# Kernel optimization log

Measured on AMD Instinct MI355X. Metric: run time of the kernel, lower is better.

Reference implementation:

```python
import jax, jax.numpy as jnp
import numpy as np

N = 400_000   # active voxels
C = 128       # inplanes = outplanes
K = 9         # nplanes*3*3 kernel offsets (nplanes=1)
EPS = 1e-4    # scn BatchNormalization default eps


def setup_inputs() -> dict:
    key = jax.random.key(0)
    ks = jax.random.split(key, 5)
    feat = jax.random.normal(ks[0], (N, C), dtype=jnp.float32)
    # rulebook: neighbor active-site index per kernel offset, plus validity mask
    nbr_idx = jax.random.randint(ks[1], (N, K), 0, N, dtype=jnp.int32)
    nbr_idx = nbr_idx.at[:, K // 2].set(jnp.arange(N, dtype=jnp.int32))  # center = self
    nbr_mask = jax.random.uniform(ks[2], (N, K)) < 0.6
    nbr_mask = nbr_mask.at[:, K // 2].set(True)
    scale = 1.0 / np.sqrt(K * C)
    W1 = jax.random.normal(ks[3], (K, C, C), dtype=jnp.float32) * scale
    W2 = jax.random.normal(ks[4], (K, C, C), dtype=jnp.float32) * scale
    gamma1 = jnp.ones((C,), jnp.float32)
    beta1 = jnp.zeros((C,), jnp.float32)
    gamma2 = jnp.ones((C,), jnp.float32)
    beta2 = jnp.zeros((C,), jnp.float32)
    return {"feat": feat, "W1": W1, "W2": W2,
            "gamma1": gamma1, "beta1": beta1,
            "gamma2": gamma2, "beta2": beta2,
            "nbr_idx": nbr_idx, "nbr_mask": nbr_mask}


def _subm_conv(feat, nbr_idx, nbr_mask, W):
    # rulebook gather -> GEMM -> accumulate; output lives at the same active sites
    out = jnp.zeros((feat.shape[0], W.shape[2]), feat.dtype)
    for k in range(W.shape[0]):  # small fixed K=9 structural loop
        xk = jnp.where(nbr_mask[:, k:k + 1], feat[nbr_idx[:, k]], 0.0)
        out = out + xk @ W[k]
    return out


def _batchnorm(x, gamma, beta):
    mu = jnp.mean(x, axis=0)
    var = jnp.mean(jnp.square(x - mu), axis=0)
    return (x - mu) * (gamma * jax.lax.rsqrt(var + EPS)) + beta


def reference(feat, W1, W2, gamma1, beta1, gamma2, beta2, nbr_idx, nbr_mask):
    residual = feat                                   # scn.Identity (stride=1)
    out = _subm_conv(feat, nbr_idx, nbr_mask, W1)     # conv1
    out = jax.nn.relu(_batchnorm(out, gamma1, beta1))  # BatchNormReLU
    out = _subm_conv(out, nbr_idx, nbr_mask, W2)      # conv2
    out = _batchnorm(out, gamma2, beta2)              # bn2
    return jax.nn.relu(out + residual)                # AddTable + ReLU
```

## Files before the change

kernel.cpp:

```cpp
#include <hip/hip_runtime.h>


#define C_CH 128
#define K_OFF 9
#define MTILE 64

typedef __attribute__((ext_vector_type(8))) short bf16x8;
typedef __attribute__((ext_vector_type(4))) float f32x4;
typedef __attribute__((ext_vector_type(8))) unsigned short u16x8;

typedef __attribute__((address_space(1))) const unsigned int* gas_p;
typedef __attribute__((address_space(3))) unsigned int* las_p;

__device__ __forceinline__ void gload_lds16(const unsigned short* g, unsigned short* l) {
    __builtin_amdgcn_global_load_lds((gas_p)g, (las_p)l, 16, 0, 0);
}

__device__ __forceinline__ unsigned short f2b(float f) {
    union { float f; unsigned u; } v; v.f = f;
    unsigned r = v.u + 0x7fffu + ((v.u >> 16) & 1u);
    return (unsigned short)(r >> 16);
}
__device__ __forceinline__ float b2f(unsigned short h) {
    union { unsigned u; float f; } v; v.u = ((unsigned)h) << 16;
    return v.f;
}


__global__ void init_k(float* stats, unsigned int* zrow1, unsigned int* zrow2) {
    int t = threadIdx.x;
    if (t < 512) stats[t] = 0.f;
    if (t >= 512 && t < 514) ((int*)stats)[1024 + (t - 512)] = 0;
    if (t < 64) { zrow1[t] = 0u; zrow2[t] = 0u; }
}

__global__ void detect_mask_k(const unsigned char* __restrict__ m, int* flagA, int* flagB) {
    int i = blockIdx.x * blockDim.x + threadIdx.x;
    unsigned char v = m[i];
    if ((i & 3) != 0 && v != 0) atomicOr(flagA, 1);
    if (v > 1) atomicOr(flagB, 1);
}

__global__ void fold_idx_k(const int* __restrict__ nidx, const void* __restrict__ m,
                           const int* __restrict__ flagA, const int* __restrict__ flagB,
                           int* __restrict__ eidx, int n, int N) {
    int i = blockIdx.x * blockDim.x + threadIdx.x;
    if (i >= n) return;
    int fa = *flagA, fb = *flagB;
    bool t;
    if (!fa)       t = ((const int*)m)[i] != 0;
    else if (fb)   t = ((const unsigned*)m)[i] != 0;
    else           t = ((const unsigned char*)m)[i] != 0;
    eidx[i] = t ? nidx[i] : N;
}

__global__ void convert_feat_k(const float* __restrict__ x, unsigned short* __restrict__ y, int n4) {
    int i = blockIdx.x * blockDim.x + threadIdx.x;
    int s = gridDim.x * blockDim.x;
    for (; i < n4; i += s) {
        float4 f = ((const float4*)x)[i];
        ushort4 o;
        o.x = f2b(f.x); o.y = f2b(f.y); o.z = f2b(f.z); o.w = f2b(f.w);
        ((ushort4*)y)[i] = o;
    }
}

__global__ void pack_w_k(const float* __restrict__ W1, unsigned short* __restrict__ Wp1,
                         const float* __restrict__ W2, unsigned short* __restrict__ Wp2) {
    int i = blockIdx.x * blockDim.x + threadIdx.x;
    const int tot = K_OFF * 8 * 4 * 512;
    const float* W = (i < tot) ? W1 : W2;
    unsigned short* Wp = (i < tot) ? Wp1 : Wp2;
    int ii = (i < tot) ? i : i - tot;
    if (i >= 2 * tot) return;
    int j = ii & 7;
    int l = (ii >> 3) & 63;
    int frag = ii >> 9;
    int ks = frag & 3;
    int nt = (frag >> 2) & 7;
    int ko = frag >> 5;
    int cin = ks * 32 + (l >> 4) * 8 + j;
    int cout = nt * 16 + (l & 15);
    Wp[ii] = f2b(W[ko * C_CH * C_CH + cin * C_CH + cout]);
}


__global__ __launch_bounds__(256) void conv_kernel(
    const unsigned short* __restrict__ Xb,
    const unsigned short* __restrict__ Wp,
    const int* __restrict__ eidx,
    unsigned short* __restrict__ Yraw,
    float* __restrict__ statS, float* __restrict__ statQ)
{
    const int tid = threadIdx.x;
    const int lane = tid & 63;
    const int wv = tid >> 6;
    const int tile = blockIdx.x * MTILE;
    const int asub = lane >> 4;
    const int l15 = lane & 15;

    __shared__ alignas(16) unsigned short At[3][MTILE * C_CH];
    __shared__ int sIdxT[K_OFF][MTILE];

    for (int i = tid; i < MTILE * K_OFF; i += 256) {
        int r = i / K_OFF, k = i - r * K_OFF;
        sIdxT[k][r] = eidx[(size_t)(tile + r) * K_OFF + k];
    }
    __syncthreads();

    const int r_st = tid >> 4;
    const int ch_st = tid & 15;

    #define STAGE(buf, ko)                                                        \
        {                                                                         \
            _Pragma("unroll")                                                     \
            for (int jr = 0; jr < 4; ++jr) {                                      \
                int r = jr * 16 + r_st;                                           \
                int g = sIdxT[ko][r];                                             \
                const unsigned short* src =                                       \
                    Xb + (size_t)g * C_CH + ((ch_st ^ (r & 7)) * 8);              \
                unsigned short* dst = &At[buf][r * C_CH + ch_st * 8];             \
                gload_lds16(src, dst);                                            \
            }                                                                     \
        }

    f32x4 acc[4][2];
    #pragma unroll
    for (int m = 0; m < 4; ++m) { acc[m][0] = (f32x4){0,0,0,0}; acc[m][1] = (f32x4){0,0,0,0}; }

    STAGE(0, 0);
    STAGE(1, 1);

    #define CONV_ITER(KO, VM)                                                     \
        {                                                                         \
            bf16x8 bfrag0[4], bfrag1[4];                                          \
            const unsigned short* wb = Wp + (size_t)(KO) * (8 * 4 * 512) + lane * 8; \
            _Pragma("unroll")                                                     \
            for (int ks = 0; ks < 4; ++ks) {                                      \
                bfrag0[ks] = *(const bf16x8*)(wb + ((wv * 2 + 0) * 4 + ks) * 512);\
                bfrag1[ks] = *(const bf16x8*)(wb + ((wv * 2 + 1) * 4 + ks) * 512);\
            }                                                                     \
            __builtin_amdgcn_sched_barrier(0);                                    \
            asm volatile("s_waitcnt vmcnt(" #VM ")" ::: "memory");                \
            __builtin_amdgcn_s_barrier();                                         \
            __builtin_amdgcn_sched_barrier(0);                                    \
            if ((KO) + 2 < K_OFF) { STAGE((((KO) + 2) % 3), (KO) + 2); }          \
            _Pragma("unroll")                                                     \
            for (int m = 0; m < 4; ++m) {                                         \
                bf16x8 a[4];                                                      \
                _Pragma("unroll")                                                 \
                for (int ks = 0; ks < 4; ++ks) {                                  \
                    int row = m * 16 + l15;                                       \
                    int sc = (ks * 4 + asub) ^ (row & 7);                         \
                    a[ks] = *(const bf16x8*)((const char*)At[(KO) % 3] + row * 256 + sc * 16); \
                }                                                                 \
                _Pragma("unroll")                                                 \
                for (int ks = 0; ks < 4; ++ks) {                                  \
                    acc[m][0] = __builtin_amdgcn_mfma_f32_16x16x32_bf16(a[ks], bfrag0[ks], acc[m][0], 0, 0, 0); \
                    acc[m][1] = __builtin_amdgcn_mfma_f32_16x16x32_bf16(a[ks], bfrag1[ks], acc[m][1], 0, 0, 0); \
                }                                                                 \
            }                                                                     \
        }

    CONV_ITER(0, 12)
    CONV_ITER(1, 20)
    CONV_ITER(2, 20)
    CONV_ITER(3, 20)
    CONV_ITER(4, 20)
    CONV_ITER(5, 20)
    CONV_ITER(6, 20)
    CONV_ITER(7, 20)
    CONV_ITER(8, 16)
    #undef CONV_ITER
    #undef STAGE

    #pragma unroll
    for (int j = 0; j < 2; ++j) {
        float s = 0.f, q = 0.f;
        #pragma unroll
        for (int m = 0; m < 4; ++m)
            #pragma unroll
            for (int r = 0; r < 4; ++r) { float v = acc[m][j][r]; s += v; q += v * v; }
        s += __shfl_xor(s, 16); s += __shfl_xor(s, 32);
        q += __shfl_xor(q, 16); q += __shfl_xor(q, 32);
        if (lane < 16) {
            atomicAdd(&statS[wv * 32 + j * 16 + lane], s);
            atomicAdd(&statQ[wv * 32 + j * 16 + lane], q);
        }
    }

    #pragma unroll
    for (int m = 0; m < 4; ++m)
        #pragma unroll
        for (int j = 0; j < 2; ++j) {
            int col = (wv * 2 + j) * 16 + l15;
            #pragma unroll
            for (int r = 0; r < 4; ++r) {
                int row = tile + m * 16 + asub * 4 + r;
                Yraw[(size_t)row * C_CH + col] = f2b(acc[m][j][r]);
            }
        }
}


__global__ void finalize_bn_k(const float* __restrict__ S, const float* __restrict__ Q,
                              const float* __restrict__ gamma, const float* __restrict__ beta,
                              float* __restrict__ scale, float* __restrict__ bias, float invN) {
    int c = threadIdx.x;
    if (c < C_CH) {
        float mu = S[c] * invN;
        float var = Q[c] * invN - mu * mu;
        float inv = rsqrtf(var + 1e-4f);
        float sc = gamma[c] * inv;
        scale[c] = sc;
        bias[c] = beta[c] - mu * sc;
    }
}

__global__ void bn_relu_k(unsigned short* __restrict__ y,
                          const float* __restrict__ scale, const float* __restrict__ bias, int n8) {
    int i0 = blockIdx.x * blockDim.x + threadIdx.x;
    int S = gridDim.x * blockDim.x;
    int c0 = (i0 * 8) & (C_CH - 1);
    float sc[8], bs[8];
    #pragma unroll
    for (int j = 0; j < 8; ++j) { sc[j] = scale[c0 + j]; bs[j] = bias[c0 + j]; }
    for (int i = i0; i < n8; i += S) {
        u16x8 v = ((const u16x8*)y)[i];
        #pragma unroll
        for (int j = 0; j < 8; ++j) {
            float x = b2f((unsigned short)v[j]);
            x = fmaxf(x * sc[j] + bs[j], 0.f);
            v[j] = (short)f2b(x);
        }
        ((u16x8*)y)[i] = v;
    }
}

__global__ void final_fuse_k(const unsigned short* __restrict__ raw,
                             const float* __restrict__ feat,
                             const float* __restrict__ scale, const float* __restrict__ bias,
                             float* __restrict__ out, int n4) {
    int i0 = blockIdx.x * blockDim.x + threadIdx.x;
    int S = gridDim.x * blockDim.x;
    int c0 = (i0 * 4) & (C_CH - 1);
    float sc[4], bs[4];
    #pragma unroll
    for (int j = 0; j < 4; ++j) { sc[j] = scale[c0 + j]; bs[j] = bias[c0 + j]; }
    for (int i = i0; i < n4; i += S) {
        ushort4 r = ((const ushort4*)raw)[i];
        float4 f = ((const float4*)feat)[i];
        float4 o;
        o.x = fmaxf(b2f(r.x) * sc[0] + bs[0] + f.x, 0.f);
        o.y = fmaxf(b2f(r.y) * sc[1] + bs[1] + f.y, 0.f);
        o.z = fmaxf(b2f(r.z) * sc[2] + bs[2] + f.z, 0.f);
        o.w = fmaxf(b2f(r.w) * sc[3] + bs[3] + f.w, 0.f);
        ((float4*)out)[i] = o;
    }
}


extern "C" void kernel_launch(void* const* d_in, const int* in_sizes, int n_in,
                              void* d_out, int out_size, void* d_ws, size_t ws_size,
                              hipStream_t stream) {
    const float* feat = (const float*)d_in[0];
    const float* W1 = (const float*)d_in[1];
    const float* W2 = (const float*)d_in[2];
    const float* g1 = (const float*)d_in[3];
    const float* b1 = (const float*)d_in[4];
    const float* g2 = (const float*)d_in[5];
    const float* b2 = (const float*)d_in[6];
    const int* nidx = (const int*)d_in[7];
    const void* nmask = d_in[8];

    const int N = in_sizes[0] / C_CH;
    const int NK = N * K_OFF;

    char* ws = (char*)d_ws;
    unsigned short* featb = (unsigned short*)ws;
    size_t off = (size_t)(N + 1) * C_CH * 2;
    off = (off + 255) & ~(size_t)255;
    unsigned short* Wp1 = (unsigned short*)(ws + off); off += (size_t)K_OFF * C_CH * C_CH * 2;
    unsigned short* Wp2 = (unsigned short*)(ws + off); off += (size_t)K_OFF * C_CH * C_CH * 2;
    float* stats = (float*)(ws + off);
    float* S1 = stats;        float* Q1 = stats + 128;
    float* S2 = stats + 256;  float* Q2 = stats + 384;
    float* sc1 = stats + 512; float* bi1 = stats + 640;
    float* sc2 = stats + 768; float* bi2 = stats + 896;
    int* flagA = ((int*)stats) + 1024;
    int* flagB = ((int*)stats) + 1025;

    unsigned short* y1 = (unsigned short*)d_out;
    int* eidx = (int*)((char*)d_out + (size_t)134217728);
    unsigned short* out2raw = featb;

    hipLaunchKernelGGL(init_k, dim3(1), dim3(514), 0, stream,
                       stats, (unsigned int*)(featb + (size_t)N * C_CH),
                       (unsigned int*)(y1 + (size_t)N * C_CH));
    hipLaunchKernelGGL(detect_mask_k, dim3(64), dim3(256), 0, stream,
                       (const unsigned char*)nmask, flagA, flagB);
    hipLaunchKernelGGL(convert_feat_k, dim3(2048), dim3(256), 0, stream, feat, featb, N * C_CH / 4);
    hipLaunchKernelGGL(pack_w_k, dim3(1152), dim3(256), 0, stream, W1, Wp1, W2, Wp2);
    hipLaunchKernelGGL(fold_idx_k, dim3((NK + 255) / 256), dim3(256), 0, stream,
                       nidx, nmask, flagA, flagB, eidx, NK, N);

    hipLaunchKernelGGL(conv_kernel, dim3(N / MTILE), dim3(256), 0, stream,
                       featb, Wp1, eidx, y1, S1, Q1);
    hipLaunchKernelGGL(finalize_bn_k, dim3(1), dim3(128), 0, stream, S1, Q1, g1, b1, sc1, bi1, 1.0f / N);
    hipLaunchKernelGGL(bn_relu_k, dim3(2048), dim3(256), 0, stream, y1, sc1, bi1, N * C_CH / 8);

    hipLaunchKernelGGL(conv_kernel, dim3(N / MTILE), dim3(256), 0, stream,
                       y1, Wp2, eidx, out2raw, S2, Q2);
    hipLaunchKernelGGL(finalize_bn_k, dim3(1), dim3(128), 0, stream, S2, Q2, g2, b2, sc2, bi2, 1.0f / N);
    hipLaunchKernelGGL(final_fuse_k, dim3(2048), dim3(256), 0, stream,
                       out2raw, feat, sc2, bi2, (float*)d_out, N * C_CH / 4);
}
```

Measured before the change: 574.3 us.

## Double conv tile to 128 rows with 8 waves, double-buffer, and fuse prep kernels

The conv kernel now processes 128 rows per block with 512 threads arranged as 2x4 waves, so each weight fragment load serves twice as many rows. The gather pipeline drops from triple to double buffering with a fixed vmcnt wait, and s_setprio is raised around the MFMA section. The small setup kernels (init, mask detect, feature convert, weight pack, index fold) are merged into two launches to cut launch overhead. Shallower prefetch may expose more gather latency, and the larger block lowers the number of resident blocks per CU.

```diff
diff --git a/kernel.cpp b/kernel.cpp
--- a/kernel.cpp
+++ b/kernel.cpp
@@ -3,7 +3,7 @@
 
 #define C_CH 128
 #define K_OFF 9
-#define MTILE 64
+#define MTILE 128
 
 typedef __attribute__((ext_vector_type(8))) short bf16x8;
 typedef __attribute__((ext_vector_type(4))) float f32x4;
@@ -27,65 +27,65 @@
 }
 
 
-__global__ void init_k(float* stats, unsigned int* zrow1, unsigned int* zrow2) {
+__global__ void init_detect_k(float* stats, unsigned int* zrow1, unsigned int* zrow2,
+                              const unsigned char* __restrict__ m, int* flagA, int* flagB) {
     int t = threadIdx.x;
-    if (t < 512) stats[t] = 0.f;
-    if (t >= 512 && t < 514) ((int*)stats)[1024 + (t - 512)] = 0;
-    if (t < 64) { zrow1[t] = 0u; zrow2[t] = 0u; }
-}
-
-__global__ void detect_mask_k(const unsigned char* __restrict__ m, int* flagA, int* flagB) {
-    int i = blockIdx.x * blockDim.x + threadIdx.x;
-    unsigned char v = m[i];
-    if ((i & 3) != 0 && v != 0) atomicOr(flagA, 1);
-    if (v > 1) atomicOr(flagB, 1);
-}
-
-__global__ void fold_idx_k(const int* __restrict__ nidx, const void* __restrict__ m,
-                           const int* __restrict__ flagA, const int* __restrict__ flagB,
-                           int* __restrict__ eidx, int n, int N) {
-    int i = blockIdx.x * blockDim.x + threadIdx.x;
-    if (i >= n) return;
+    if (blockIdx.x == 0) {
+        if (t < 256) { stats[t] = 0.f; stats[256 + t] = 0.f; }
+        if (t >= 256 && t < 258) ((int*)stats)[1024 + (t - 256)] = 0;
+        if (t < 64) { zrow1[t] = 0u; zrow2[t] = 0u; }
+    } else {
+        int i = (blockIdx.x - 1) * 256 + t;
+        unsigned char v = m[i];
+        if ((i & 3) != 0 && v != 0) atomicOr(flagA, 1);
+        if (v > 1) atomicOr(flagB, 1);
+    }
+}
+
+__global__ void prep_k(const float* __restrict__ x, unsigned short* __restrict__ y, int n4,
+                       const float* __restrict__ W1, unsigned short* __restrict__ Wp1,
+                       const float* __restrict__ W2, unsigned short* __restrict__ Wp2,
+                       const int* __restrict__ nidx, const void* __restrict__ m,
+                       const int* __restrict__ flagA, const int* __restrict__ flagB,
+                       int* __restrict__ eidx, int NK, int N) {
+    const int PACK = K_OFF * 8 * 4 * 512;
     int fa = *flagA, fb = *flagB;
-    bool t;
-    if (!fa)       t = ((const int*)m)[i] != 0;
-    else if (fb)   t = ((const unsigned*)m)[i] != 0;
-    else           t = ((const unsigned char*)m)[i] != 0;
-    eidx[i] = t ? nidx[i] : N;
-}
-
-__global__ void convert_feat_k(const float* __restrict__ x, unsigned short* __restrict__ y, int n4) {
     int i = blockIdx.x * blockDim.x + threadIdx.x;
     int s = gridDim.x * blockDim.x;
-    for (; i < n4; i += s) {
-        float4 f = ((const float4*)x)[i];
-        ushort4 o;
-        o.x = f2b(f.x); o.y = f2b(f.y); o.z = f2b(f.z); o.w = f2b(f.w);
-        ((ushort4*)y)[i] = o;
-    }
-}
-
-__global__ void pack_w_k(const float* __restrict__ W1, unsigned short* __restrict__ Wp1,
-                         const float* __restrict__ W2, unsigned short* __restrict__ Wp2) {
-    int i = blockIdx.x * blockDim.x + threadIdx.x;
-    const int tot = K_OFF * 8 * 4 * 512;
-    const float* W = (i < tot) ? W1 : W2;
-    unsigned short* Wp = (i < tot) ? Wp1 : Wp2;
-    int ii = (i < tot) ? i : i - tot;
-    if (i >= 2 * tot) return;
-    int j = ii & 7;
-    int l = (ii >> 3) & 63;
-    int frag = ii >> 9;
-    int ks = frag & 3;
-    int nt = (frag >> 2) & 7;
-    int ko = frag >> 5;
-    int cin = ks * 32 + (l >> 4) * 8 + j;
-    int cout = nt * 16 + (l & 15);
-    Wp[ii] = f2b(W[ko * C_CH * C_CH + cin * C_CH + cout]);
-}
-
-
-__global__ __launch_bounds__(256) void conv_kernel(
+    int tot = n4 + 2 * PACK + NK;
+    for (; i < tot; i += s) {
+        if (i < n4) {
+            float4 f = ((const float4*)x)[i];
+            ushort4 o;
+            o.x = f2b(f.x); o.y = f2b(f.y); o.z = f2b(f.z); o.w = f2b(f.w);
+            ((ushort4*)y)[i] = o;
+        } else if (i < n4 + 2 * PACK) {
+            int ii = i - n4;
+            const float* W = (ii < PACK) ? W1 : W2;
+            unsigned short* Wp = (ii < PACK) ? Wp1 : Wp2;
+            if (ii >= PACK) ii -= PACK;
+            int j = ii & 7;
+            int l = (ii >> 3) & 63;
+            int frag = ii >> 9;
+            int ks = frag & 3;
+            int nt = (frag >> 2) & 7;
+            int ko = frag >> 5;
+            int cin = ks * 32 + (l >> 4) * 8 + j;
+            int cout = nt * 16 + (l & 15);
+            Wp[ii] = f2b(W[ko * C_CH * C_CH + cin * C_CH + cout]);
+        } else {
+            int j = i - n4 - 2 * PACK;
+            bool t;
+            if (!fa)       t = ((const int*)m)[j] != 0;
+            else if (fb)   t = ((const unsigned*)m)[j] != 0;
+            else           t = ((const unsigned char*)m)[j] != 0;
+            eidx[j] = t ? nidx[j] : N;
+        }
+    }
+}
+
+
+__global__ __launch_bounds__(512) void conv_kernel(
     const unsigned short* __restrict__ Xb,
     const unsigned short* __restrict__ Wp,
     const int* __restrict__ eidx,
@@ -95,14 +95,16 @@
     const int tid = threadIdx.x;
     const int lane = tid & 63;
     const int wv = tid >> 6;
+    const int wr = wv >> 2;
+    const int wc = wv & 3;
     const int tile = blockIdx.x * MTILE;
     const int asub = lane >> 4;
     const int l15 = lane & 15;
 
-    __shared__ alignas(16) unsigned short At[3][MTILE * C_CH];
+    __shared__ alignas(16) unsigned short At[2][MTILE * C_CH];
     __shared__ int sIdxT[K_OFF][MTILE];
 
-    for (int i = tid; i < MTILE * K_OFF; i += 256) {
+    for (int i = tid; i < MTILE * K_OFF; i += 512) {
         int r = i / K_OFF, k = i - r * K_OFF;
         sIdxT[k][r] = eidx[(size_t)(tile + r) * K_OFF + k];
     }
@@ -115,7 +117,7 @@
         {                                                                         \
             _Pragma("unroll")                                                     \
             for (int jr = 0; jr < 4; ++jr) {                                      \
-                int r = jr * 16 + r_st;                                           \
+                int r = jr * 32 + r_st;                                           \
                 int g = sIdxT[ko][r];                                             \
                 const unsigned short* src =                                       \
                     Xb + (size_t)g * C_CH + ((ch_st ^ (r & 7)) * 8);              \
@@ -129,30 +131,30 @@
     for (int m = 0; m < 4; ++m) { acc[m][0] = (f32x4){0,0,0,0}; acc[m][1] = (f32x4){0,0,0,0}; }
 
     STAGE(0, 0);
-    STAGE(1, 1);
-
-    #define CONV_ITER(KO, VM)                                                     \
+
+    #define CONV_ITER(KO)                                                         \
         {                                                                         \
             bf16x8 bfrag0[4], bfrag1[4];                                          \
             const unsigned short* wb = Wp + (size_t)(KO) * (8 * 4 * 512) + lane * 8; \
             _Pragma("unroll")                                                     \
             for (int ks = 0; ks < 4; ++ks) {                                      \
-                bfrag0[ks] = *(const bf16x8*)(wb + ((wv * 2 + 0) * 4 + ks) * 512);\
-                bfrag1[ks] = *(const bf16x8*)(wb + ((wv * 2 + 1) * 4 + ks) * 512);\
+                bfrag0[ks] = *(const bf16x8*)(wb + ((wc * 2 + 0) * 4 + ks) * 512);\
+                bfrag1[ks] = *(const bf16x8*)(wb + ((wc * 2 + 1) * 4 + ks) * 512);\
             }                                                                     \
             __builtin_amdgcn_sched_barrier(0);                                    \
-            asm volatile("s_waitcnt vmcnt(" #VM ")" ::: "memory");                \
+            asm volatile("s_waitcnt vmcnt(8)" ::: "memory");                      \
             __builtin_amdgcn_s_barrier();                                         \
             __builtin_amdgcn_sched_barrier(0);                                    \
-            if ((KO) + 2 < K_OFF) { STAGE((((KO) + 2) % 3), (KO) + 2); }          \
+            if ((KO) + 1 < K_OFF) { STAGE((((KO) + 1) & 1), (KO) + 1); }          \
+            __builtin_amdgcn_s_setprio(1);                                        \
             _Pragma("unroll")                                                     \
             for (int m = 0; m < 4; ++m) {                                         \
                 bf16x8 a[4];                                                      \
                 _Pragma("unroll")                                                 \
                 for (int ks = 0; ks < 4; ++ks) {                                  \
-                    int row = m * 16 + l15;                                       \
+                    int row = wr * 64 + m * 16 + l15;                             \
                     int sc = (ks * 4 + asub) ^ (row & 7);                         \
-                    a[ks] = *(const bf16x8*)((const char*)At[(KO) % 3] + row * 256 + sc * 16); \
+                    a[ks] = *(const bf16x8*)((const char*)At[(KO) & 1] + row * 256 + sc * 16); \
                 }                                                                 \
                 _Pragma("unroll")                                                 \
                 for (int ks = 0; ks < 4; ++ks) {                                  \
@@ -160,17 +162,18 @@
                     acc[m][1] = __builtin_amdgcn_mfma_f32_16x16x32_bf16(a[ks], bfrag1[ks], acc[m][1], 0, 0, 0); \
                 }                                                                 \
             }                                                                     \
-        }
-
-    CONV_ITER(0, 12)
-    CONV_ITER(1, 20)
-    CONV_ITER(2, 20)
-    CONV_ITER(3, 20)
-    CONV_ITER(4, 20)
-    CONV_ITER(5, 20)
-    CONV_ITER(6, 20)
-    CONV_ITER(7, 20)
-    CONV_ITER(8, 16)
+            __builtin_amdgcn_s_setprio(0);                                        \
+        }
+
+    CONV_ITER(0)
+    CONV_ITER(1)
+    CONV_ITER(2)
+    CONV_ITER(3)
+    CONV_ITER(4)
+    CONV_ITER(5)
+    CONV_ITER(6)
+    CONV_ITER(7)
+    CONV_ITER(8)
     #undef CONV_ITER
     #undef STAGE
 
@@ -184,8 +187,8 @@
         s += __shfl_xor(s, 16); s += __shfl_xor(s, 32);
         q += __shfl_xor(q, 16); q += __shfl_xor(q, 32);
         if (lane < 16) {
-            atomicAdd(&statS[wv * 32 + j * 16 + lane], s);
-            atomicAdd(&statQ[wv * 32 + j * 16 + lane], q);
+            atomicAdd(&statS[wc * 32 + j * 16 + lane], s);
+            atomicAdd(&statQ[wc * 32 + j * 16 + lane], q);
         }
     }
 
@@ -193,10 +196,10 @@
     for (int m = 0; m < 4; ++m)
         #pragma unroll
         for (int j = 0; j < 2; ++j) {
-            int col = (wv * 2 + j) * 16 + l15;
+            int col = (wc * 2 + j) * 16 + l15;
             #pragma unroll
             for (int r = 0; r < 4; ++r) {
-                int row = tile + m * 16 + asub * 4 + r;
+                int row = tile + wr * 64 + m * 16 + asub * 4 + r;
                 Yraw[(size_t)row * C_CH + col] = f2b(acc[m][j][r]);
             }
         }
@@ -294,22 +297,21 @@
     int* eidx = (int*)((char*)d_out + (size_t)134217728);
     unsigned short* out2raw = featb;
 
-    hipLaunchKernelGGL(init_k, dim3(1), dim3(514), 0, stream,
+    hipLaunchKernelGGL(init_detect_k, dim3(65), dim3(256), 0, stream,
                        stats, (unsigned int*)(featb + (size_t)N * C_CH),
-                       (unsigned int*)(y1 + (size_t)N * C_CH));
-    hipLaunchKernelGGL(detect_mask_k, dim3(64), dim3(256), 0, stream,
+                       (unsigned int*)(y1 + (size_t)N * C_CH),
                        (const unsigned char*)nmask, flagA, flagB);
-    hipLaunchKernelGGL(convert_feat_k, dim3(2048), dim3(256), 0, stream, feat, featb, N * C_CH / 4);
-    hipLaunchKernelGGL(pack_w_k, dim3(1152), dim3(256), 0, stream, W1, Wp1, W2, Wp2);
-    hipLaunchKernelGGL(fold_idx_k, dim3((NK + 255) / 256), dim3(256), 0, stream,
+    hipLaunchKernelGGL(prep_k, dim3(2048), dim3(256), 0, stream,
+                       feat, featb, N * C_CH / 4,
+                       W1, Wp1, W2, Wp2,
                        nidx, nmask, flagA, flagB, eidx, NK, N);
 
-    hipLaunchKernelGGL(conv_kernel, dim3(N / MTILE), dim3(256), 0, stream,
+    hipLaunchKernelGGL(conv_kernel, dim3(N / MTILE), dim3(512), 0, stream,
                        featb, Wp1, eidx, y1, S1, Q1);
     hipLaunchKernelGGL(finalize_bn_k, dim3(1), dim3(128), 0, stream, S1, Q1, g1, b1, sc1, bi1, 1.0f / N);
     hipLaunchKernelGGL(bn_relu_k, dim3(2048), dim3(256), 0, stream, y1, sc1, bi1, N * C_CH / 8);
 
-    hipLaunchKernelGGL(conv_kernel, dim3(N / MTILE), dim3(256), 0, stream,
+    hipLaunchKernelGGL(conv_kernel, dim3(N / MTILE), dim3(512), 0, stream,
                        y1, Wp2, eidx, out2raw, S2, Q2);
     hipLaunchKernelGGL(finalize_bn_k, dim3(1), dim3(128), 0, stream, S2, Q2, g2, b2, sc2, bi2, 1.0f / N);
     hipLaunchKernelGGL(final_fuse_k, dim3(2048), dim3(256), 0, stream,
```

New measurement: 604.9 us. 1.05x slower.
